# Performance work log

Hardware: AMD Instinct MI355X
Metric: run time of the kernel (lower is better)

## Reference

```python
import jax, jax.numpy as jnp
import numpy as np

SHAPES = ((100, 152), (50, 76), (25, 38), (13, 19))  # per-level (H, W), stride 8/16/32/64 of 800x1216
S_TOTAL = sum(h * w for h, w in SHAPES)  # 20197
D, H, LVL, P, NL, H2 = 256, 8, 4, 4, 6, 2
B, NQ_TOTAL, NPROP = 8, 350, 300
DFF = 1024


def layer_norm(x, w, b, eps=1e-5):
    m = jnp.mean(x, -1, keepdims=True)
    v = jnp.mean((x - m) ** 2, -1, keepdims=True)
    return (x - m) / jnp.sqrt(v + eps) * w + b


def pos2posemb(pos, num_pos_feats=64, temperature=10000.0):
    pos = pos * (2.0 * np.pi)
    dim_t = temperature ** (2.0 * (jnp.arange(num_pos_feats) // 2).astype(jnp.float32) / num_pos_feats)
    pe = pos[..., None] / dim_t  # [..., 4, 64]
    pe = jnp.stack((jnp.sin(pe[..., 0::2]), jnp.cos(pe[..., 1::2])), axis=-1)  # [..., 4, 32, 2]
    return pe.reshape(pe.shape[:-3] + (-1,))  # [..., 256]


def bilinear_gather(v_l, loc, hl, wl):
    # v_l [B, hl*wl, H, Dh]; loc [B, Nq, H, P, 2] in [0,1]; grid_sample align_corners=False, zero padding
    b, nq, h, p, _ = loc.shape
    dh = v_l.shape[-1]
    x = loc[..., 0] * wl - 0.5
    y = loc[..., 1] * hl - 0.5
    x0 = jnp.floor(x)
    y0 = jnp.floor(y)
    lx = x - x0
    ly = y - y0

    def g(xi, yi):
        valid = (xi >= 0) & (xi <= wl - 1) & (yi >= 0) & (yi <= hl - 1)
        xi_i = jnp.clip(xi, 0, wl - 1).astype(jnp.int32)
        yi_i = jnp.clip(yi, 0, hl - 1).astype(jnp.int32)
        idx = (yi_i * wl + xi_i).transpose(0, 1, 3, 2).reshape(b, nq * p, h)  # per-head spatial index
        out = jnp.take_along_axis(v_l, jnp.broadcast_to(idx[..., None], (b, nq * p, h, dh)), axis=1)
        out = out.reshape(b, nq, p, h, dh).transpose(0, 1, 3, 2, 4)  # [B,Nq,H,P,Dh]
        return out * valid.astype(v_l.dtype)[..., None]

    return (g(x0, y0) * ((1 - lx) * (1 - ly))[..., None]
            + g(x0 + 1, y0) * (lx * (1 - ly))[..., None]
            + g(x0, y0 + 1) * ((1 - lx) * ly)[..., None]
            + g(x0 + 1, y0 + 1) * (lx * ly)[..., None])


def ms_deform_attn(query, ref, src, Woff, boff, Wa, ba, Wv, bv, Wout, bout):
    b, nq, d = query.shape
    dh = d // H
    value = (src @ Wv + bv).reshape(b, -1, H, dh)
    off = (query @ Woff + boff).reshape(b, nq, H, LVL, P, 2)
    attn = jax.nn.softmax((query @ Wa + ba).reshape(b, nq, H, LVL * P), -1).reshape(b, nq, H, LVL, P)
    # 4-d reference points: center + offsets scaled by box size
    loc = ref[:, :, None, :, None, :2] + off / P * ref[:, :, None, :, None, 2:] * 0.5  # [b,nq,H,L,P,2]
    out = jnp.zeros((b, nq, H, dh), query.dtype)
    start = 0
    for l, (hl, wl) in enumerate(SHAPES):
        v_l = value[:, start:start + hl * wl]
        start += hl * wl
        samp = bilinear_gather(v_l, loc[:, :, :, l], hl, wl)  # [b,nq,H,P,dh]
        out = out + (samp * attn[:, :, :, l, :, None]).sum(3)
    return out.reshape(b, nq, d) @ Wout + bout


def weight_attn(q_in, k_in, Wq, bq, Wk, bk):
    b, nq, d = q_in.shape
    nk = k_in.shape[1]
    dh = d // H2
    q = (q_in @ Wq + bq).reshape(b, nq, H2, dh).transpose(0, 2, 1, 3)
    k = (k_in @ Wk + bk).reshape(b, nk, H2, dh).transpose(0, 2, 1, 3)
    mm = jax.nn.softmax(jnp.einsum('bhqd,bhkd->bhqk', q, k) * (1.0 / dh ** 0.5), -1)
    qn = q / (jnp.linalg.norm(q, axis=-1, keepdims=True) + 1e-6)
    kn = k / (jnp.linalg.norm(k, axis=-1, keepdims=True) + 1e-6)
    cos = jnp.einsum('bhqd,bhkd->bhqk', qn, kn)
    return cos, mm


def setup_inputs():
    key = jax.random.key(0)
    ks = jax.random.split(key, 32)
    f = jnp.float32
    inp = {}
    inp['tgt'] = jax.random.normal(ks[0], (B, NQ_TOTAL, D), f)
    inp['reference_points'] = jax.random.uniform(ks[1], (B, NQ_TOTAL, 4), f, 0.05, 0.95)
    inp['src'] = jax.random.normal(ks[2], (B, S_TOTAL, D), f)
    inp['src_spatial_shapes'] = jnp.array(SHAPES, jnp.int32)
    lsi = np.cumsum([0] + [h * w for h, w in SHAPES])[:-1]
    inp['src_level_start_index'] = jnp.array(lsi, jnp.int32)
    inp['src_valid_ratios'] = jnp.ones((B, LVL, 2), f)
    inp['num_proposals'] = NPROP
    names = [('Woff', (NL, D, H * LVL * P * 2)), ('boff', (NL, H * LVL * P * 2)),
             ('Wa', (NL, D, H * LVL * P)), ('ba', (NL, H * LVL * P)),
             ('Wv', (NL, D, D)), ('bv', (NL, D)), ('Wout', (NL, D, D)), ('bout', (NL, D)),
             ('Wl1', (NL, D, DFF)), ('bl1', (NL, DFF)), ('Wl2', (NL, DFF, D)), ('bl2', (NL, D)),
             ('Wq', (NL, D, D)), ('bq', (NL, D)), ('Wk', (NL, D, D)), ('bk', (NL, D))]
    for i, (n, s) in enumerate(names):
        inp[n] = jax.random.normal(ks[3 + i], s, f) * 0.02
    inp['n1w'] = jnp.ones((NL, D), f)
    inp['n1b'] = jnp.zeros((NL, D), f)
    inp['n3w'] = jnp.ones((NL, D), f)
    inp['n3b'] = jnp.zeros((NL, D), f)
    return inp


def reference(tgt, reference_points, src, src_spatial_shapes, src_level_start_index,
              src_valid_ratios, num_proposals, Woff, boff, Wa, ba, Wv, bv, Wout, bout,
              Wl1, bl1, Wl2, bl2, Wq, bq, Wk, bk, n1w, n1b, n3w, n3b):
    proposals = tgt[:, :num_proposals]
    track_queries = tgt[:, num_proposals:]
    p_ref = reference_points[:, :num_proposals]
    t_ref = reference_points[:, num_proposals:]
    vr = jnp.concatenate([src_valid_ratios, src_valid_ratios], -1)  # [B,L,4]
    ref_input = p_ref[:, :, None] * vr[:, None]  # [B,Np,L,4]
    p_pos = pos2posemb(p_ref)
    t_pos = pos2posemb(t_ref)  # computed per torch code; WeightAttention ignores pos
    for l in range(NL):
        q = proposals + p_pos
        ca = ms_deform_attn(q, ref_input, src, Woff[l], boff[l], Wa[l], ba[l], Wv[l], bv[l], Wout[l], bout[l])
        proposals = layer_norm(proposals + ca, n1w[l], n1b[l])  # dropout = identity (eval)
        ffn = jax.nn.relu(proposals @ Wl1[l] + bl1[l]) @ Wl2[l] + bl2[l]
        proposals = layer_norm(proposals + ffn, n3w[l], n3b[l])
        pt_cos, pt_mm = weight_attn(proposals, track_queries, Wq[l], bq[l], Wk[l], bk[l])
        pp_cos, pp_mm = weight_attn(proposals, proposals, Wq[l], bq[l], Wk[l], bk[l])
    return proposals, p_ref, pt_cos, pp_cos, pt_mm, pp_mm
```

## Files before the change

kernel.cpp:

```cpp
#include <hip/hip_runtime.h>

#define BB 8
#define NQ 300
#define NTQ 50
#define NLAY 6
#define S_TOTAL 20197
#define ROWS (BB*NQ)
#define MVAL (BB*S_TOTAL)

typedef unsigned short u16;
typedef unsigned int u32;
typedef __bf16 v8bf __attribute__((ext_vector_type(8)));
typedef float f32x4 __attribute__((ext_vector_type(4)));

__device__ __forceinline__ u16 f2b(float f) {
    u32 u = __float_as_uint(f);
    u32 r = (u + 0x7fffu + ((u >> 16) & 1u)) >> 16;
    return (u16)r;
}
__device__ __forceinline__ u32 pk2(float lo, float hi) {
    return (u32)f2b(lo) | ((u32)f2b(hi) << 16);
}

#define ASYNC_CP16(dst_lds, src_g) \
    __builtin_amdgcn_global_load_lds((const __attribute__((address_space(1))) u32*)(src_g), \
                                     (__attribute__((address_space(3))) u32*)(dst_lds), 16, 0, 0)

__global__ void transpose_pack(
    const float* Woff, const float* Wa, const float* Wv, const float* Wout,
    const float* Wl1, const float* Wl2, const float* Wq, const float* Wk,
    const float* boff, const float* ba, const float* bvp, const float* bout,
    const float* bl1, const float* bl2, const float* bq, const float* bk,
    u16* wt, float* bias)
{
    int idx = blockIdx.x * 256 + threadIdx.x;
    if (idx < 5308416) {
        int l = idx / 884736;
        int o = idx % 884736;
        float v;
        if (o < 98304) { int n = o >> 8, k = o & 255;
            v = (n < 256) ? Woff[l*65536 + k*256 + n] : Wa[l*32768 + k*128 + (n-256)];
        } else if (o < 163840) { int o2 = o - 98304; int n = o2 >> 8, k = o2 & 255;
            v = Wv[l*65536 + k*256 + n];
        } else if (o < 229376) { int o2 = o - 163840; int n = o2 >> 8, k = o2 & 255;
            v = Wout[l*65536 + k*256 + n];
        } else if (o < 491520) { int o2 = o - 229376; int n = o2 >> 8, k = o2 & 255;
            v = Wl1[l*262144 + k*1024 + n];
        } else if (o < 753664) { int o2 = o - 491520; int n = o2 >> 10, k = o2 & 1023;
            v = Wl2[l*262144 + k*256 + n];
        } else { int o2 = o - 753664; int n = o2 >> 8, k = o2 & 255;
            v = (n < 256) ? Wq[l*65536 + k*256 + n] : Wk[l*65536 + k*256 + (n-256)];
        }
        wt[idx] = f2b(v);
    } else {
        int i2 = idx - 5308416;
        if (i2 < 16128) {
            int l = i2 / 2688, o = i2 % 2688;
            float v;
            if (o < 256)       v = boff[l*256 + o];
            else if (o < 384)  v = ba  [l*128 + (o-256)];
            else if (o < 640)  v = bvp [l*256 + (o-384)];
            else if (o < 896)  v = bout[l*256 + (o-640)];
            else if (o < 1920) v = bl1 [l*1024 + (o-896)];
            else if (o < 2176) v = bl2 [l*256 + (o-1920)];
            else if (o < 2432) v = bq  [l*256 + (o-2176)];
            else               v = bk  [l*256 + (o-2432)];
            bias[i2] = v;
        }
    }
}

__global__ void setup_kernel(const float* tgt, const float* refp, float* prop,
                             u16* q_b, float* ppos, u16* tq, float* out_pref)
{
    int row = blockIdx.x, t = threadIdx.x;
    if (row < ROWS) {
        int b = row / NQ, q = row % NQ;
        int k = t >> 6, rem = t & 63, j = rem >> 1;
        float pr = refp[(b*350 + q)*4 + k];
        float dimt = powf(10000.0f, (float)j * (1.0f/32.0f));
        float arg = pr * 6.283185307179586f / dimt;
        float pe = (rem & 1) ? cosf(arg) : sinf(arg);
        ppos[row*256 + t] = pe;
        float pv = tgt[(b*350 + q)*256 + t];
        prop[row*256 + t] = pv;
        q_b[row*256 + t] = f2b(pv + pe);
        if (t < 4) out_pref[row*4 + t] = refp[(b*350 + q)*4 + t];
    } else {
        int r2 = row - ROWS;
        int b = r2 / NTQ, qq = r2 % NTQ;
        tq[r2*256 + t] = f2b(tgt[(b*350 + NQ + qq)*256 + t]);
    }
}

__global__ __launch_bounds__(256) void gemm_bt64(
    const u16* __restrict__ A, const u16* __restrict__ Bt,
    const float* __restrict__ bias, void* __restrict__ Cout,
    int M, int N, int K, int flags)
{
    __shared__ __align__(16) u16 As[2][64*32];
    __shared__ __align__(16) u16 Bs[2][128*32];
    int tid = threadIdx.x;
    int lane = tid & 63, wave = tid >> 6;
    int bm = blockIdx.y * 64, bn = blockIdx.x * 128;
    int wm = (wave >> 1) * 32, wn = (wave & 1) * 64;
    f32x4 acc[2][4] = {};
    int r = tid >> 2, c = (tid & 3) * 8;
    const u16* Ap0 = A  + (long)min(bm + r,      M-1) * K + c;
    const u16* Bp0 = Bt + (long)min(bn + r,      N-1) * K + c;
    const u16* Bp1 = Bt + (long)min(bn + r + 64, N-1) * K + c;
    int fr = lane & 15, fk = (lane >> 4) * 8;

    auto STG = [&](int bi, int k0) {
        ASYNC_CP16(&As[bi][tid*8],         Ap0 + k0);
        ASYNC_CP16(&Bs[bi][tid*8],         Bp0 + k0);
        ASYNC_CP16(&Bs[bi][64*32 + tid*8], Bp1 + k0);
    };
    STG(0, 0);
    asm volatile("s_waitcnt vmcnt(0)" ::: "memory");
    __syncthreads();
    int cur = 0;
    for (int k0 = 0; k0 < K; k0 += 32) {
        if (k0 + 32 < K) STG(cur ^ 1, k0 + 32);
        v8bf af[2], bf[4];
        #pragma unroll
        for (int i = 0; i < 2; ++i) af[i] = *(const v8bf*)&As[cur][(wm + i*16 + fr)*32 + fk];
        #pragma unroll
        for (int j = 0; j < 4; ++j) bf[j] = *(const v8bf*)&Bs[cur][(wn + j*16 + fr)*32 + fk];
        #pragma unroll
        for (int i = 0; i < 2; ++i)
            #pragma unroll
            for (int j = 0; j < 4; ++j)
                acc[i][j] = __builtin_amdgcn_mfma_f32_16x16x32_bf16(af[i], bf[j], acc[i][j], 0, 0, 0);
        asm volatile("s_waitcnt vmcnt(0)" ::: "memory");
        __syncthreads();
        cur ^= 1;
    }
    int cq = lane >> 4, cn = lane & 15;
    #pragma unroll
    for (int i = 0; i < 2; ++i) {
        #pragma unroll
        for (int j = 0; j < 4; ++j) {
            int col = bn + wn + j*16 + cn;
            float bv_ = bias ? bias[col] : 0.0f;
            #pragma unroll
            for (int rr = 0; rr < 4; ++rr) {
                int m = bm + wm + i*16 + cq*4 + rr;
                if (m < M) {
                    float v = acc[i][j][rr] + bv_;
                    if (flags & 1) v = fmaxf(v, 0.0f);
                    if (flags & 2) ((u16*)Cout)[(long)m*N + col] = f2b(v);
                    else           ((float*)Cout)[(long)m*N + col] = v;
                }
            }
        }
    }
}

__global__ __launch_bounds__(256, 2) void gemm_value6_v5(
    const float* __restrict__ srcf, const u16* __restrict__ wtall,
    const float* __restrict__ biasall, u16* __restrict__ Cout)
{
    __shared__ __align__(16) u16 Bsw[8*4*128*8];
    __shared__ __align__(16) u16 scr[4][16*40];
    int tid = threadIdx.x;
    int lane = tid & 63, wave = tid >> 6;
    int fr = lane & 15, q = lane >> 4;
    long rowb = (long)blockIdx.x * 128 + wave*32;

    const float* Ar0 = srcf + (long)min(rowb + fr,      (long)(MVAL-1))*256 + q*8;
    const float* Ar1 = srcf + (long)min(rowb + 16 + fr, (long)(MVAL-1))*256 + q*8;
    v8bf a0[8], a1[8];
    #pragma unroll
    for (int ks = 0; ks < 8; ++ks) {
        float4 lo = *(const float4*)(Ar0 + ks*32);
        float4 hi = *(const float4*)(Ar0 + ks*32 + 4);
        uint4 pk = make_uint4(pk2(lo.x,lo.y), pk2(lo.z,lo.w), pk2(hi.x,hi.y), pk2(hi.z,hi.w));
        a0[ks] = *(v8bf*)&pk;
        float4 lo1 = *(const float4*)(Ar1 + ks*32);
        float4 hi1 = *(const float4*)(Ar1 + ks*32 + 4);
        uint4 pk1 = make_uint4(pk2(lo1.x,lo1.y), pk2(lo1.z,lo1.w), pk2(hi1.x,hi1.y), pk2(hi1.z,hi1.w));
        a1[ks] = *(v8bf*)&pk1;
    }

    u16* myscr = &scr[wave][0];
    int rlane = lane >> 2;
    int clane = (lane & 3) * 8;

    for (int t = 0; t < 12; ++t) {
        int z = t >> 1, half = t & 1;
        const u16* Bt = wtall + (size_t)z*884736 + 98304 + (size_t)(half*128)*256;
        if (t) __syncthreads();
        #pragma unroll
        for (int it = 0; it < 16; ++it) {
            int c_id = it*256 + tid;
            int col = c_id & 127, chunk = (c_id >> 7) & 3, ks = c_id >> 9;
            ASYNC_CP16(&Bsw[(size_t)c_id*8], Bt + (size_t)col*256 + ks*32 + chunk*8);
        }
        asm volatile("s_waitcnt vmcnt(0)" ::: "memory");
        __syncthreads();

        u16* Cz = Cout + (size_t)z*((size_t)MVAL*256);
        const float* bs = biasall + z*2688 + 384 + half*128;

        f32x4 acc0[8] = {}, acc1[8] = {};
        #pragma unroll
        for (int ks = 0; ks < 8; ++ks) {
            v8bf bf[8];
            #pragma unroll
            for (int j = 0; j < 8; ++j)
                bf[j] = *(const v8bf*)&Bsw[ks*4096 + q*1024 + (j*16 + fr)*8];
            #pragma unroll
            for (int j = 0; j < 8; ++j) {
                acc0[j] = __builtin_amdgcn_mfma_f32_16x16x32_bf16(a0[ks], bf[j], acc0[j], 0, 0, 0);
                acc1[j] = __builtin_amdgcn_mfma_f32_16x16x32_bf16(a1[ks], bf[j], acc1[j], 0, 0, 0);
            }
        }
        #pragma unroll
        for (int p = 0; p < 4; ++p) {
            float blo = bs[p*32 + fr];
            float bhi = bs[p*32 + 16 + fr];
            #pragma unroll
            for (int rr = 0; rr < 4; ++rr) {
                myscr[(q*4+rr)*40 + fr]      = f2b(acc0[2*p][rr]   + blo);
                myscr[(q*4+rr)*40 + 16 + fr] = f2b(acc0[2*p+1][rr] + bhi);
            }
            asm volatile("s_waitcnt lgkmcnt(0)" ::: "memory");
            __builtin_amdgcn_sched_barrier(0);
            uint4 v0 = *(const uint4*)&myscr[rlane*40 + clane];
            asm volatile("s_waitcnt lgkmcnt(0)" ::: "memory");
            __builtin_amdgcn_sched_barrier(0);
            long g0 = rowb + rlane;
            if (g0 < MVAL)
                *(uint4*)&Cz[g0*256 + half*128 + p*32 + clane] = v0;
            #pragma unroll
            for (int rr = 0; rr < 4; ++rr) {
                myscr[(q*4+rr)*40 + fr]      = f2b(acc1[2*p][rr]   + blo);
                myscr[(q*4+rr)*40 + 16 + fr] = f2b(acc1[2*p+1][rr] + bhi);
            }
            asm volatile("s_waitcnt lgkmcnt(0)" ::: "memory");
            __builtin_amdgcn_sched_barrier(0);
            uint4 v1 = *(const uint4*)&myscr[rlane*40 + clane];
            asm volatile("s_waitcnt lgkmcnt(0)" ::: "memory");
            __builtin_amdgcn_sched_barrier(0);
            long g1 = rowb + 16 + rlane;
            if (g1 < MVAL)
                *(uint4*)&Cz[g1*256 + half*128 + p*32 + clane] = v1;
        }
    }
}

__global__ __launch_bounds__(256) void sample_fused(
    const u16* __restrict__ value, const float* __restrict__ offatt,
    const float* __restrict__ refp, const float* __restrict__ svr,
    u16* __restrict__ sampout)
{
    int row = blockIdx.x, t = threadIdx.x;
    int b = row / NQ, q = row % NQ;
    __shared__ float lg[128], awl[128], sxl[128], syl[128];
    const int WL[4] = {152,76,38,19}, HL[4] = {100,50,25,13}, LS[4] = {0,15200,19000,19950};

    if (t < 128) lg[t] = offatt[row*384 + 256 + t];
    __syncthreads();
    if (t < 128) {
        int h = t >> 4, s = t & 15, lvl = s >> 2, pp = s & 3;
        int gb = h << 4;
        float mx = -1e30f;
        for (int i = 0; i < 16; ++i) mx = fmaxf(mx, lg[gb + i]);
        float sm = 0.f;
        for (int i = 0; i < 16; ++i) sm += expf(lg[gb + i] - mx);
        awl[t] = expf(lg[t] - mx) / sm;
        float rx = refp[(b*350+q)*4 + 0] * svr[(b*4+lvl)*2 + 0];
        float ry = refp[(b*350+q)*4 + 1] * svr[(b*4+lvl)*2 + 1];
        float rw = refp[(b*350+q)*4 + 2] * svr[(b*4+lvl)*2 + 0];
        float rh = refp[(b*350+q)*4 + 3] * svr[(b*4+lvl)*2 + 1];
        float ox = offatt[row*384 + h*32 + lvl*8 + pp*2 + 0];
        float oy = offatt[row*384 + h*32 + lvl*8 + pp*2 + 1];
        sxl[t] = (rx + ox * 0.25f * rw * 0.5f) * (float)WL[lvl] - 0.5f;
        syl[t] = (ry + oy * 0.25f * rh * 0.5f) * (float)HL[lvl] - 0.5f;
    }
    __syncthreads();

    int lane = t & 63, wv = t >> 6;
    int g = lane >> 3, e = lane & 7;
    for (int hh = 0; hh < 2; ++hh) {
        int h = wv*2 + hh;
        float a0 = 0.f, a1 = 0.f, a2 = 0.f, a3 = 0.f;
        #pragma unroll
        for (int it = 0; it < 8; ++it) {
            int task = it*8 + g;
            int s = task >> 2, cc = task & 3;
            int cx = cc & 1, cy = cc >> 1;
            int lvl = s >> 2;
            float x = sxl[h*16 + s], y2 = syl[h*16 + s], aw = awl[h*16 + s];
            float x0 = floorf(x), y0 = floorf(y2);
            float xc = x0 + (float)cx, yc = y0 + (float)cy;
            int wl = WL[lvl], hl = HL[lvl];
            if (xc >= 0.f && xc <= (float)(wl-1) && yc >= 0.f && yc <= (float)(hl-1)) {
                float lx = x - x0, ly = y2 - y0;
                float wgt = aw * (cx ? lx : 1.f - lx) * (cy ? ly : 1.f - ly);
                long off = ((long)b*S_TOTAL + LS[lvl] + (int)yc*wl + (int)xc)*256 + h*32 + e*4;
                uint2 v = *(const uint2*)(value + off);
                a0 += wgt * __uint_as_float((v.x & 0xffffu) << 16);
                a1 += wgt * __uint_as_float(v.x & 0xffff0000u);
                a2 += wgt * __uint_as_float((v.y & 0xffffu) << 16);
                a3 += wgt * __uint_as_float(v.y & 0xffff0000u);
            }
        }
        #pragma unroll
        for (int o = 8; o < 64; o <<= 1) {
            a0 += __shfl_xor(a0, o); a1 += __shfl_xor(a1, o);
            a2 += __shfl_xor(a2, o); a3 += __shfl_xor(a3, o);
        }
        if (g == 0)
            *(uint2*)&sampout[row*256 + h*32 + e*4] = make_uint2(pk2(a0, a1), pk2(a2, a3));
    }
}

__global__ void ln_kernel(float* __restrict__ prop, const float* __restrict__ delta,
                          const float* __restrict__ w, const float* __restrict__ bsh,
                          u16* __restrict__ pb_out, u16* __restrict__ q_out,
                          const float* __restrict__ ppos)
{
    int row = blockIdx.x, t = threadIdx.x;
    int lane = t & 63, wv = t >> 6;
    float v = prop[row*256 + t] + delta[row*256 + t];
    float s = v;
    for (int o = 32; o; o >>= 1) s += __shfl_xor(s, o);
    __shared__ float red[4], red2[4];
    if (lane == 0) red[wv] = s;
    __syncthreads();
    float mean = (red[0]+red[1]+red[2]+red[3]) * (1.0f/256.0f);
    float dd = v - mean;
    float s2 = dd * dd;
    for (int o = 32; o; o >>= 1) s2 += __shfl_xor(s2, o);
    if (lane == 0) red2[wv] = s2;
    __syncthreads();
    float var = (red2[0]+red2[1]+red2[2]+red2[3]) * (1.0f/256.0f);
    float nv = dd * rsqrtf(var + 1e-5f) * w[t] + bsh[t];
    prop[row*256 + t] = nv;
    pb_out[row*256 + t] = f2b(nv);
    if (q_out) q_out[row*256 + t] = f2b(nv + ppos[row*256 + t]);
}

__global__ __launch_bounds__(128) void qk_convert(
    const float* __restrict__ qkp, const float* __restrict__ kt,
    u16* __restrict__ qk_b, u16* __restrict__ kt_b,
    float* __restrict__ qn_g, float* __restrict__ knp_g, float* __restrict__ knt_g)
{
    int row = blockIdx.x, t = threadIdx.x;
    __shared__ float part[128];
    if (row < ROWS) {
        const float* sp = qkp + (long)row*512 + t*4;
        float4 v = *(const float4*)sp;
        *(uint2*)&qk_b[(long)row*512 + t*4] = make_uint2(pk2(v.x,v.y), pk2(v.z,v.w));
        part[t] = v.x*v.x + v.y*v.y + v.z*v.z + v.w*v.w;
        __syncthreads();
        if (t < 4) {
            float s = 0.f;
            for (int i = 0; i < 32; ++i) s += part[t*32 + i];
            int b = row / NQ, q = row % NQ;
            float nv = sqrtf(s) + 1e-6f;
            if      (t == 0) qn_g [(b*2+0)*NQ + q] = nv;
            else if (t == 1) qn_g [(b*2+1)*NQ + q] = nv;
            else if (t == 2) knp_g[(b*2+0)*NQ + q] = nv;
            else             knp_g[(b*2+1)*NQ + q] = nv;
        }
    } else {
        int r2 = row - ROWS;
        float ss = 0.f;
        if (t < 64) {
            const float* sp = kt + (long)r2*256 + t*4;
            float4 v = *(const float4*)sp;
            *(uint2*)&kt_b[(long)r2*256 + t*4] = make_uint2(pk2(v.x,v.y), pk2(v.z,v.w));
            ss = v.x*v.x + v.y*v.y + v.z*v.z + v.w*v.w;
        }
        part[t] = ss;
        __syncthreads();
        if (t < 2) {
            float s = 0.f;
            for (int i = 0; i < 32; ++i) s += part[t*32 + i];
            int b = r2 / NTQ, qq = r2 % NTQ;
            knt_g[(b*2+t)*NTQ + qq] = sqrtf(s) + 1e-6f;
        }
    }
}

__global__ __launch_bounds__(256) void wattn_mfma(
    const u16* __restrict__ Qb, const u16* __restrict__ Kb,
    int qstride, int kstride, int koff, int nk,
    const float* __restrict__ qn_g, const float* __restrict__ kn_g,
    float* __restrict__ out_cos, float* __restrict__ out_logit)
{
    __shared__ __align__(16) u16 As[2][128*32];
    __shared__ __align__(16) u16 Bs[2][128*32];
    int bh = blockIdx.z, b = bh >> 1, h = bh & 1;
    int tid = threadIdx.x;
    int lane = tid & 63, wave = tid >> 6;
    int bm = blockIdx.y * 128, bn = blockIdx.x * 128;
    int wm = (wave >> 1) * 64, wn = (wave & 1) * 64;
    f32x4 acc[4][4] = {};
    int r = tid >> 2, c = (tid & 3) * 8;
    const u16* Ap0 = Qb + (long)(b*NQ + min(bm + r,      NQ-1))*qstride + h*128 + c;
    const u16* Ap1 = Qb + (long)(b*NQ + min(bm + r + 64, NQ-1))*qstride + h*128 + c;
    const u16* Bp0 = Kb + (long)(b*nk + min(bn + r,      nk-1))*kstride + koff + h*128 + c;
    const u16* Bp1 = Kb + (long)(b*nk + min(bn + r + 64, nk-1))*kstride + koff + h*128 + c;
    int fr = lane & 15, fk = (lane >> 4) * 8;

    auto STG = [&](int bi, int k0) {
        ASYNC_CP16(&As[bi][tid*8],         Ap0 + k0);
        ASYNC_CP16(&As[bi][64*32 + tid*8], Ap1 + k0);
        ASYNC_CP16(&Bs[bi][tid*8],         Bp0 + k0);
        ASYNC_CP16(&Bs[bi][64*32 + tid*8], Bp1 + k0);
    };
    STG(0, 0);
    asm volatile("s_waitcnt vmcnt(0)" ::: "memory");
    __syncthreads();
    int cur = 0;
    for (int k0 = 0; k0 < 128; k0 += 32) {
        if (k0 + 32 < 128) STG(cur ^ 1, k0 + 32);
        v8bf af[4], bf[4];
        #pragma unroll
        for (int i = 0; i < 4; ++i) af[i] = *(const v8bf*)&As[cur][(wm + i*16 + fr)*32 + fk];
        #pragma unroll
        for (int j = 0; j < 4; ++j) bf[j] = *(const v8bf*)&Bs[cur][(wn + j*16 + fr)*32 + fk];
        #pragma unroll
        for (int i = 0; i < 4; ++i)
            #pragma unroll
            for (int j = 0; j < 4; ++j)
                acc[i][j] = __builtin_amdgcn_mfma_f32_16x16x32_bf16(af[i], bf[j], acc[i][j], 0, 0, 0);
        asm volatile("s_waitcnt vmcnt(0)" ::: "memory");
        __syncthreads();
        cur ^= 1;
    }
    const float SC = 0.08838834764831845f;
    int cq = lane >> 4, cn = lane & 15;
    #pragma unroll
    for (int i = 0; i < 4; ++i) {
        #pragma unroll
        for (int j = 0; j < 4; ++j) {
            int col = bn + wn + j*16 + cn;
            #pragma unroll
            for (int rr = 0; rr < 4; ++rr) {
                int m = bm + wm + i*16 + cq*4 + rr;
                if (m < NQ && col < nk) {
                    float d = acc[i][j][rr];
                    long o = ((long)(bh*NQ + m))*nk + col;
                    out_cos[o]   = d / (qn_g[bh*NQ + m] * kn_g[bh*nk + col]);
                    out_logit[o] = d * SC;
                }
            }
        }
    }
}

__global__ __launch_bounds__(64) void row_softmax(float* __restrict__ buf, int nk)
{
    long row = blockIdx.x;
    float* p = buf + row*nk;
    int lane = threadIdx.x;
    float mx = -1e30f;
    for (int k = lane; k < nk; k += 64) mx = fmaxf(mx, p[k]);
    for (int o = 32; o; o >>= 1) mx = fmaxf(mx, __shfl_xor(mx, o));
    float s = 0.f;
    for (int k = lane; k < nk; k += 64) s += expf(p[k] - mx);
    for (int o = 32; o; o >>= 1) s += __shfl_xor(s, o);
    float inv = 1.0f / s;
    for (int k = lane; k < nk; k += 64) p[k] = expf(p[k] - mx) * inv;
}

__global__ void writeout_kernel(const float* __restrict__ prop, float* __restrict__ out)
{
    int row = blockIdx.x, t = threadIdx.x;
    out[row*256 + t] = prop[row*256 + t];
}

extern "C" void kernel_launch(void* const* d_in, const int* in_sizes, int n_in,
                              void* d_out, int out_size, void* d_ws, size_t ws_size,
                              hipStream_t stream)
{
    (void)in_sizes; (void)n_in; (void)out_size; (void)ws_size;
    const float* tgt  = (const float*)d_in[0];
    const float* refp = (const float*)d_in[1];
    const float* src  = (const float*)d_in[2];
    const float* svr  = (const float*)d_in[5];
    const float* Woff = (const float*)d_in[7];
    const float* boff = (const float*)d_in[8];
    const float* Wa   = (const float*)d_in[9];
    const float* ba   = (const float*)d_in[10];
    const float* Wv   = (const float*)d_in[11];
    const float* bv   = (const float*)d_in[12];
    const float* Wout = (const float*)d_in[13];
    const float* bout = (const float*)d_in[14];
    const float* Wl1  = (const float*)d_in[15];
    const float* bl1  = (const float*)d_in[16];
    const float* Wl2  = (const float*)d_in[17];
    const float* bl2  = (const float*)d_in[18];
    const float* Wq   = (const float*)d_in[19];
    const float* bq   = (const float*)d_in[20];
    const float* Wk   = (const float*)d_in[21];
    const float* bk   = (const float*)d_in[22];
    const float* n1w  = (const float*)d_in[23];
    const float* n1b  = (const float*)d_in[24];
    const float* n3w  = (const float*)d_in[25];
    const float* n3b  = (const float*)d_in[26];
    float* out = (float*)d_out;

    char* p = (char*)d_ws;
    auto alloc = [&](size_t bytes) { void* r = (void*)p; p += (bytes + 255) & ~(size_t)255; return r; };
    u16*   wt      = (u16*)  alloc(6ull*884736*2);
    float* bias    = (float*)alloc(6ull*2688*4);
    u16*   value   = (u16*)  alloc(6ull*MVAL*256*2);
    float* prop    = (float*)alloc((size_t)ROWS*256*4);
    u16*   prop_b  = (u16*)  alloc((size_t)ROWS*256*2);
    u16*   q_b     = (u16*)  alloc((size_t)ROWS*256*2);
    float* ppos    = (float*)alloc((size_t)ROWS*256*4);
    float* offatt  = (float*)alloc((size_t)ROWS*384*4);
    u16*   sampout = (u16*)  alloc((size_t)ROWS*256*2);
    float* ca      = (float*)alloc((size_t)ROWS*256*4);
    u16*   ff1     = (u16*)  alloc((size_t)ROWS*1024*2);
    float* ff2     = (float*)alloc((size_t)ROWS*256*4);
    u16*   tq      = (u16*)  alloc(400ull*256*2);
    float* qkp     = (float*)alloc((size_t)ROWS*512*4);
    float* kt      = (float*)alloc(400ull*256*4);
    u16*   qk_b    = (u16*)  alloc((size_t)ROWS*512*2);
    u16*   kt_b    = (u16*)  alloc(400ull*256*2);
    float* qn_g    = (float*)alloc(16ull*NQ*4);
    float* knp_g   = (float*)alloc(16ull*NQ*4);
    float* knt_g   = (float*)alloc(16ull*NTQ*4);

    transpose_pack<<<20799, 256, 0, stream>>>(Woff, Wa, Wv, Wout, Wl1, Wl2, Wq, Wk,
                                              boff, ba, bv, bout, bl1, bl2, bq, bk, wt, bias);
    setup_kernel<<<ROWS + 400, 256, 0, stream>>>(tgt, refp, prop, q_b, ppos, tq, out + 614400);
    gemm_value6_v5<<<1263, 256, 0, stream>>>(src, wt, bias, value);

    for (int l = 0; l < NLAY; ++l) {
        const u16* wl_ = wt + (size_t)l*884736;
        const float* bl_ = bias + l*2688;
        gemm_bt64<<<dim3(3, 38), 256, 0, stream>>>(q_b,    wl_,          bl_,        offatt, ROWS, 384, 256, 0);
        sample_fused<<<ROWS, 256, 0, stream>>>(value + (size_t)l*MVAL*256, offatt, refp, svr, sampout);
        gemm_bt64<<<dim3(2, 38), 256, 0, stream>>>(sampout, wl_ + 163840, bl_ + 640,  ca,    ROWS, 256, 256, 0);
        ln_kernel<<<ROWS, 256, 0, stream>>>(prop, ca, n1w + l*256, n1b + l*256, prop_b, (u16*)nullptr, ppos);
        gemm_bt64<<<dim3(8, 38), 256, 0, stream>>>(prop_b, wl_ + 229376, bl_ + 896,  ff1,   ROWS, 1024, 256, 3);
        gemm_bt64<<<dim3(2, 38), 256, 0, stream>>>(ff1,    wl_ + 491520, bl_ + 1920, ff2,   ROWS, 256, 1024, 0);
        ln_kernel<<<ROWS, 256, 0, stream>>>(prop, ff2, n3w + l*256, n3b + l*256, prop_b, q_b, ppos);
    }

    const u16* w5 = wt + 5ull*884736;
    const float* b5 = bias + 5*2688;
    gemm_bt64<<<dim3(4, 38), 256, 0, stream>>>(prop_b, w5 + 753664,         b5 + 2176,       qkp, ROWS, 512, 256, 0);
    gemm_bt64<<<dim3(2, 7),  256, 0, stream>>>(tq,     w5 + 753664 + 65536, b5 + 2176 + 256, kt,  400,  256, 256, 0);
    qk_convert<<<2800, 128, 0, stream>>>(qkp, kt, qk_b, kt_b, qn_g, knp_g, knt_g);
    wattn_mfma<<<dim3(1, 3, 16), 256, 0, stream>>>(qk_b, kt_b, 512, 256, 0,   NTQ, qn_g, knt_g,
                                                   out + 624000, out + 2304000);
    wattn_mfma<<<dim3(3, 3, 16), 256, 0, stream>>>(qk_b, qk_b, 512, 512, 256, NQ,  qn_g, knp_g,
                                                   out + 864000, out + 2544000);
    row_softmax<<<4800, 64, 0, stream>>>(out + 2304000, NTQ);
    row_softmax<<<4800, 64, 0, stream>>>(out + 2544000, NQ);
    writeout_kernel<<<ROWS, 256, 0, stream>>>(prop, out);
}
```

Baseline: 1.207 ms.

## Fuse output/FFN2 GEMMs with residual LayerNorm and double-buffer value GEMM weights

Adds a gemm_ln kernel that computes a full 256-wide output row block per workgroup, adds bias and residual, and performs LayerNorm in the epilogue. This replaces the separate out-projection/FFN2 GEMMs plus ln_kernel and removes the ca/ff2 intermediate buffers and two launches per layer. The value-projection GEMM now splits N into 64-column groups and double-buffers the weight tile in LDS, so loading the next tile overlaps with the MFMAs on the current one. The cost is that the fused GEMM runs only 38 workgroups, which leaves most of the GPU idle, especially for the K=1024 FFN2.

```diff
diff --git a/kernel.cpp b/kernel.cpp
--- a/kernel.cpp
+++ b/kernel.cpp
@@ -157,11 +157,124 @@
     }
 }
 
-__global__ __launch_bounds__(256, 2) void gemm_value6_v5(
+__global__ __launch_bounds__(256) void gemm_ln(
+    const u16* __restrict__ A, const u16* __restrict__ Bt,
+    const float* __restrict__ bias, int K,
+    float* __restrict__ prop, const float* __restrict__ lnw,
+    const float* __restrict__ lnb, u16* __restrict__ pb_out,
+    u16* __restrict__ q_out, const float* __restrict__ ppos)
+{
+    __shared__ __align__(16) u16 As[2][64*32];
+    __shared__ __align__(16) u16 Bs[2][256*32];
+    __shared__ float redS[64][2], redQ[64][2];
+    int tid = threadIdx.x;
+    int lane = tid & 63, wave = tid >> 6;
+    int bm = blockIdx.x * 64;
+    int wm = (wave >> 1) * 32, wn = (wave & 1) * 128;
+    f32x4 acc[2][8] = {};
+    int fr = lane & 15, fk = (lane >> 4) * 8, q = lane >> 4;
+
+    int ar = tid >> 2, ac = (tid & 3) * 8;
+    const u16* Ap = A + (long)min(bm + ar, ROWS-1) * K + ac;
+    auto STG = [&](int bi, int k0) {
+        ASYNC_CP16(&As[bi][tid*8], Ap + k0);
+        #pragma unroll
+        for (int it = 0; it < 4; ++it) {
+            int c_id = it*256 + tid;
+            ASYNC_CP16(&Bs[bi][(size_t)c_id*8], Bt + (long)(c_id >> 2)*K + k0 + (c_id & 3)*8);
+        }
+    };
+    STG(0, 0);
+    asm volatile("s_waitcnt vmcnt(0)" ::: "memory");
+    __syncthreads();
+    int cur = 0;
+    for (int k0 = 0; k0 < K; k0 += 32) {
+        if (k0 + 32 < K) STG(cur ^ 1, k0 + 32);
+        v8bf af[2], bf[8];
+        #pragma unroll
+        for (int i = 0; i < 2; ++i) af[i] = *(const v8bf*)&As[cur][(wm + i*16 + fr)*32 + fk];
+        #pragma unroll
+        for (int j = 0; j < 8; ++j) bf[j] = *(const v8bf*)&Bs[cur][(wn + j*16 + fr)*32 + fk];
+        #pragma unroll
+        for (int i = 0; i < 2; ++i)
+            #pragma unroll
+            for (int j = 0; j < 8; ++j)
+                acc[i][j] = __builtin_amdgcn_mfma_f32_16x16x32_bf16(af[i], bf[j], acc[i][j], 0, 0, 0);
+        asm volatile("s_waitcnt vmcnt(0)" ::: "memory");
+        __syncthreads();
+        cur ^= 1;
+    }
+
+    #pragma unroll
+    for (int i = 0; i < 2; ++i)
+        #pragma unroll
+        for (int j = 0; j < 8; ++j) {
+            int col = wn + j*16 + fr;
+            float bv_ = bias[col];
+            #pragma unroll
+            for (int rr = 0; rr < 4; ++rr) {
+                int m = min(bm + wm + i*16 + q*4 + rr, ROWS-1);
+                acc[i][j][rr] += bv_ + prop[(long)m*256 + col];
+            }
+        }
+    float s1[2][4];
+    #pragma unroll
+    for (int i = 0; i < 2; ++i)
+        #pragma unroll
+        for (int rr = 0; rr < 4; ++rr) {
+            float s = 0.f;
+            #pragma unroll
+            for (int j = 0; j < 8; ++j) s += acc[i][j][rr];
+            for (int mk = 1; mk < 16; mk <<= 1) s += __shfl_xor(s, mk);
+            s1[i][rr] = s;
+            if (fr == 0) redS[wm + i*16 + q*4 + rr][wave & 1] = s;
+        }
+    __syncthreads();
+    float mean[2][4];
+    #pragma unroll
+    for (int i = 0; i < 2; ++i)
+        #pragma unroll
+        for (int rr = 0; rr < 4; ++rr) {
+            int rl = wm + i*16 + q*4 + rr;
+            mean[i][rr] = (redS[rl][0] + redS[rl][1]) * (1.0f/256.0f);
+        }
+    #pragma unroll
+    for (int i = 0; i < 2; ++i)
+        #pragma unroll
+        for (int rr = 0; rr < 4; ++rr) {
+            float s = 0.f;
+            #pragma unroll
+            for (int j = 0; j < 8; ++j) { float d = acc[i][j][rr] - mean[i][rr]; s += d*d; }
+            for (int mk = 1; mk < 16; mk <<= 1) s += __shfl_xor(s, mk);
+            if (fr == 0) redQ[wm + i*16 + q*4 + rr][wave & 1] = s;
+        }
+    __syncthreads();
+    #pragma unroll
+    for (int i = 0; i < 2; ++i)
+        #pragma unroll
+        for (int rr = 0; rr < 4; ++rr) {
+            int rl = wm + i*16 + q*4 + rr;
+            float var = (redQ[rl][0] + redQ[rl][1]) * (1.0f/256.0f);
+            float rstd = rsqrtf(var + 1e-5f);
+            int m = bm + rl;
+            if (m < ROWS) {
+                #pragma unroll
+                for (int j = 0; j < 8; ++j) {
+                    int col = wn + j*16 + fr;
+                    float nv = (acc[i][j][rr] - mean[i][rr]) * rstd * lnw[col] + lnb[col];
+                    prop[(long)m*256 + col] = nv;
+                    pb_out[(long)m*256 + col] = f2b(nv);
+                    if (q_out) q_out[(long)m*256 + col] = f2b(nv + ppos[(long)m*256 + col]);
+                }
+            }
+        }
+}
+
+__global__ __launch_bounds__(256, 2) void gemm_value6_v6(
     const float* __restrict__ srcf, const u16* __restrict__ wtall,
     const float* __restrict__ biasall, u16* __restrict__ Cout)
 {
-    __shared__ __align__(16) u16 Bsw[8*4*128*8];
+    __shared__ __align__(16) u16 Bsw[2][8*2048];
     __shared__ __align__(16) u16 scr[4][16*40];
     int tid = threadIdx.x;
     int lane = tid & 63, wave = tid >> 6;
@@ -183,41 +296,46 @@
         a1[ks] = *(v8bf*)&pk1;
     }
 
+    auto STG = [&](int bi, int t2) {
+        int z = t2 >> 2, g = t2 & 3;
+        const u16* Bt = wtall + (size_t)z*884736 + 98304 + (size_t)(g*64)*256;
+        #pragma unroll
+        for (int it = 0; it < 8; ++it) {
+            int c_id = it*256 + tid;
+            int col = c_id & 63, chunk = (c_id >> 6) & 3, ks = c_id >> 8;
+            ASYNC_CP16(&Bsw[bi][(size_t)c_id*8], Bt + (size_t)col*256 + ks*32 + chunk*8);
+        }
+    };
+    STG(0, 0);
+    asm volatile("s_waitcnt vmcnt(0)" ::: "memory");
+    __syncthreads();
+
     u16* myscr = &scr[wave][0];
     int rlane = lane >> 2;
     int clane = (lane & 3) * 8;
 
-    for (int t = 0; t < 12; ++t) {
-        int z = t >> 1, half = t & 1;
-        const u16* Bt = wtall + (size_t)z*884736 + 98304 + (size_t)(half*128)*256;
-        if (t) __syncthreads();
-        #pragma unroll
-        for (int it = 0; it < 16; ++it) {
-            int c_id = it*256 + tid;
-            int col = c_id & 127, chunk = (c_id >> 7) & 3, ks = c_id >> 9;
-            ASYNC_CP16(&Bsw[(size_t)c_id*8], Bt + (size_t)col*256 + ks*32 + chunk*8);
-        }
-        asm volatile("s_waitcnt vmcnt(0)" ::: "memory");
-        __syncthreads();
-
+    int buf = 0;
+    for (int t2 = 0; t2 < 24; ++t2) {
+        if (t2 + 1 < 24) STG(buf ^ 1, t2 + 1);
+        int z = t2 >> 2, g = t2 & 3;
         u16* Cz = Cout + (size_t)z*((size_t)MVAL*256);
-        const float* bs = biasall + z*2688 + 384 + half*128;
-
-        f32x4 acc0[8] = {}, acc1[8] = {};
+        const float* bs = biasall + z*2688 + 384 + g*64;
+
+        f32x4 acc0[4] = {}, acc1[4] = {};
         #pragma unroll
         for (int ks = 0; ks < 8; ++ks) {
-            v8bf bf[8];
-            #pragma unroll
-            for (int j = 0; j < 8; ++j)
-                bf[j] = *(const v8bf*)&Bsw[ks*4096 + q*1024 + (j*16 + fr)*8];
-            #pragma unroll
-            for (int j = 0; j < 8; ++j) {
+            v8bf bf[4];
+            #pragma unroll
+            for (int j = 0; j < 4; ++j)
+                bf[j] = *(const v8bf*)&Bsw[buf][ks*2048 + q*512 + (j*16 + fr)*8];
+            #pragma unroll
+            for (int j = 0; j < 4; ++j) {
                 acc0[j] = __builtin_amdgcn_mfma_f32_16x16x32_bf16(a0[ks], bf[j], acc0[j], 0, 0, 0);
                 acc1[j] = __builtin_amdgcn_mfma_f32_16x16x32_bf16(a1[ks], bf[j], acc1[j], 0, 0, 0);
             }
         }
         #pragma unroll
-        for (int p = 0; p < 4; ++p) {
+        for (int p = 0; p < 2; ++p) {
             float blo = bs[p*32 + fr];
             float bhi = bs[p*32 + 16 + fr];
             #pragma unroll
@@ -232,7 +350,7 @@
             __builtin_amdgcn_sched_barrier(0);
             long g0 = rowb + rlane;
             if (g0 < MVAL)
-                *(uint4*)&Cz[g0*256 + half*128 + p*32 + clane] = v0;
+                *(uint4*)&Cz[g0*256 + g*64 + p*32 + clane] = v0;
             #pragma unroll
             for (int rr = 0; rr < 4; ++rr) {
                 myscr[(q*4+rr)*40 + fr]      = f2b(acc1[2*p][rr]   + blo);
@@ -245,8 +363,11 @@
             __builtin_amdgcn_sched_barrier(0);
             long g1 = rowb + 16 + rlane;
             if (g1 < MVAL)
-                *(uint4*)&Cz[g1*256 + half*128 + p*32 + clane] = v1;
-        }
+                *(uint4*)&Cz[g1*256 + g*64 + p*32 + clane] = v1;
+        }
+        asm volatile("s_waitcnt vmcnt(0)" ::: "memory");
+        __syncthreads();
+        buf ^= 1;
     }
 }
 
@@ -315,32 +436,6 @@
         if (g == 0)
             *(uint2*)&sampout[row*256 + h*32 + e*4] = make_uint2(pk2(a0, a1), pk2(a2, a3));
     }
-}
-
-__global__ void ln_kernel(float* __restrict__ prop, const float* __restrict__ delta,
-                          const float* __restrict__ w, const float* __restrict__ bsh,
-                          u16* __restrict__ pb_out, u16* __restrict__ q_out,
-                          const float* __restrict__ ppos)
-{
-    int row = blockIdx.x, t = threadIdx.x;
-    int lane = t & 63, wv = t >> 6;
-    float v = prop[row*256 + t] + delta[row*256 + t];
-    float s = v;
-    for (int o = 32; o; o >>= 1) s += __shfl_xor(s, o);
-    __shared__ float red[4], red2[4];
-    if (lane == 0) red[wv] = s;
-    __syncthreads();
-    float mean = (red[0]+red[1]+red[2]+red[3]) * (1.0f/256.0f);
-    float dd = v - mean;
-    float s2 = dd * dd;
-    for (int o = 32; o; o >>= 1) s2 += __shfl_xor(s2, o);
-    if (lane == 0) red2[wv] = s2;
-    __syncthreads();
-    float var = (red2[0]+red2[1]+red2[2]+red2[3]) * (1.0f/256.0f);
-    float nv = dd * rsqrtf(var + 1e-5f) * w[t] + bsh[t];
-    prop[row*256 + t] = nv;
-    pb_out[row*256 + t] = f2b(nv);
-    if (q_out) q_out[row*256 + t] = f2b(nv + ppos[row*256 + t]);
 }
 
 __global__ __launch_bounds__(128) void qk_convert(
@@ -517,9 +612,7 @@
     float* ppos    = (float*)alloc((size_t)ROWS*256*4);
     float* offatt  = (float*)alloc((size_t)ROWS*384*4);
     u16*   sampout = (u16*)  alloc((size_t)ROWS*256*2);
-    float* ca      = (float*)alloc((size_t)ROWS*256*4);
     u16*   ff1     = (u16*)  alloc((size_t)ROWS*1024*2);
-    float* ff2     = (float*)alloc((size_t)ROWS*256*4);
     u16*   tq      = (u16*)  alloc(400ull*256*2);
     float* qkp     = (float*)alloc((size_t)ROWS*512*4);
     float* kt      = (float*)alloc(400ull*256*4);
@@ -532,18 +625,20 @@
     transpose_pack<<<20799, 256, 0, stream>>>(Woff, Wa, Wv, Wout, Wl1, Wl2, Wq, Wk,
                                               boff, ba, bv, bout, bl1, bl2, bq, bk, wt, bias);
     setup_kernel<<<ROWS + 400, 256, 0, stream>>>(tgt, refp, prop, q_b, ppos, tq, out + 614400);
-    gemm_value6_v5<<<1263, 256, 0, stream>>>(src, wt, bias, value);
+    gemm_value6_v6<<<1263, 256, 0, stream>>>(src, wt, bias, value);
 
     for (int l = 0; l < NLAY; ++l) {
         const u16* wl_ = wt + (size_t)l*884736;
         const float* bl_ = bias + l*2688;
         gemm_bt64<<<dim3(3, 38), 256, 0, stream>>>(q_b,    wl_,          bl_,        offatt, ROWS, 384, 256, 0);
         sample_fused<<<ROWS, 256, 0, stream>>>(value + (size_t)l*MVAL*256, offatt, refp, svr, sampout);
-        gemm_bt64<<<dim3(2, 38), 256, 0, stream>>>(sampout, wl_ + 163840, bl_ + 640,  ca,    ROWS, 256, 256, 0);
-        ln_kernel<<<ROWS, 256, 0, stream>>>(prop, ca, n1w + l*256, n1b + l*256, prop_b, (u16*)nullptr, ppos);
+        gemm_ln<<<38, 256, 0, stream>>>(sampout, wl_ + 163840, bl_ + 640, 256,
+                                        prop, n1w + l*256, n1b + l*256, prop_b,
+                                        (u16*)nullptr, (const float*)nullptr);
         gemm_bt64<<<dim3(8, 38), 256, 0, stream>>>(prop_b, wl_ + 229376, bl_ + 896,  ff1,   ROWS, 1024, 256, 3);
-        gemm_bt64<<<dim3(2, 38), 256, 0, stream>>>(ff1,    wl_ + 491520, bl_ + 1920, ff2,   ROWS, 256, 1024, 0);
-        ln_kernel<<<ROWS, 256, 0, stream>>>(prop, ff2, n3w + l*256, n3b + l*256, prop_b, q_b, ppos);
+        gemm_ln<<<38, 256, 0, stream>>>(ff1, wl_ + 491520, bl_ + 1920, 1024,
+                                        prop, n3w + l*256, n3b + l*256, prop_b,
+                                        q_b, ppos);
     }
 
     const u16* w5 = wt + 5ull*884736;
```

Result: slower. 1.427 ms (+18.2%).
